# Optimization experiments

Measured on AMD Instinct MI355X. Metric: run time of the kernel, lower is better.

The kernel has to match this reference:

```python
import jax, jax.numpy as jnp
import numpy as np

B, S, D = 2, 192, 256


def _clip_tangent(v, max_norm=4.0):
    n = jnp.linalg.norm(v, axis=-1, keepdims=True) + 1e-8
    return v * jnp.minimum(max_norm / n, 1.0)


def _sq(x):
    return jnp.sum(x * x, axis=-1, keepdims=True)


def _artanh(x):
    return jnp.arctanh(jnp.clip(x, -1.0 + 1e-7, 1.0 - 1e-7))


def _mobius_add(x, y):
    # Poincare ball (c=1) Mobius addition
    x2, y2 = _sq(x), _sq(y)
    xy = jnp.sum(x * y, axis=-1, keepdims=True)
    num = (1.0 + 2.0 * xy + y2) * x + (1.0 - x2) * y
    den = 1.0 + 2.0 * xy + x2 * y2
    return num / jnp.maximum(den, 1e-15)


def _expmap0(v):
    n = jnp.maximum(jnp.linalg.norm(v, axis=-1, keepdims=True), 1e-15)
    return jnp.tanh(n) * v / n


def _logmap0(x):
    n = jnp.maximum(jnp.linalg.norm(x, axis=-1, keepdims=True), 1e-15)
    return _artanh(n) * x / n


def _dist(x, y):
    u = _mobius_add(-x, y)
    return 2.0 * _artanh(jnp.linalg.norm(u, axis=-1))


def _logmap(x, y):
    u = _mobius_add(-x, y)
    un = jnp.maximum(jnp.linalg.norm(u, axis=-1, keepdims=True), 1e-15)
    lam = 2.0 / jnp.maximum(1.0 - _sq(x), 1e-15)
    return (2.0 / lam) * _artanh(un) * u / un


def _expmap(x, v):
    n = jnp.maximum(jnp.linalg.norm(v, axis=-1, keepdims=True), 1e-15)
    lam = 2.0 / jnp.maximum(1.0 - _sq(x), 1e-15)
    return _mobius_add(x, jnp.tanh(lam * n / 2.0) * v / n)


def _projx(x):
    n = jnp.linalg.norm(x, axis=-1, keepdims=True)
    maxn = 1.0 - 1e-5
    return jnp.where(n > maxn, x * maxn / jnp.maximum(n, 1e-15), x)


def _normalize(v, axis, eps=1e-8):
    return v / jnp.maximum(jnp.linalg.norm(v, axis=axis, keepdims=True), eps)


def setup_inputs() -> dict:
    key = jax.random.key(0)
    ks = jax.random.split(key, 8)

    def lin_w(k):
        return 0.02 * jax.random.normal(k, (D, D), jnp.float32)

    return {
        'q_in': 0.1 * jax.random.normal(ks[0], (B, S, D), jnp.float32),
        'k_in': 0.1 * jax.random.normal(ks[1], (B, S, D), jnp.float32),
        'v_in': 0.1 * jax.random.normal(ks[2], (B, S, D), jnp.float32),
        'Wq': lin_w(ks[3]), 'bq': jnp.zeros((D,), jnp.float32),
        'Wk': lin_w(ks[4]), 'bk': jnp.zeros((D,), jnp.float32),
        'Wv': lin_w(ks[5]), 'bv': jnp.zeros((D,), jnp.float32),
        'Wo': lin_w(ks[6]), 'bo': jnp.zeros((D,), jnp.float32),
        'tau': jnp.asarray(0.02, jnp.float32),
        'tangent_scale': jnp.asarray(1.0, jnp.float32),
    }


def _forward(q_in, k_in, v_in, Wq, bq, Wk, bk, Wv, bv, Wo, bo, tau, tangent_scale):
    nk = jax.random.split(jax.random.key(42), 3)  # deterministic stand-in for randn_like noise
    q = q_in @ Wq.T + bq
    k = k_in @ Wk.T + bk
    v = v_in @ Wv.T + bv

    q_hyp = _expmap0(_clip_tangent(q))
    k_hyp = _expmap0(_clip_tangent(k))

    # pairwise hyperbolic distance attention: [B,S,S]
    dist_matrix = _dist(q_hyp[:, :, None, :], k_hyp[:, None, :, :])
    min_dist = jnp.min(dist_matrix, axis=-1, keepdims=True)
    w_unnorm = jnp.exp(-(dist_matrix - min_dist))
    w_probs = w_unnorm / (jnp.sum(w_unnorm, axis=-1, keepdims=True) + 1e-8)
    h = jnp.einsum('bqs,bsd->bqd', w_probs, v)

    # differentiable Karcher flow (3-step Riemannian SGD for Frechet mean)
    wn = w_unnorm / (jnp.sum(w_unnorm, axis=-1, keepdims=True) + 1e-8)
    mu_hyp = _expmap0(_clip_tangent(jnp.einsum('bqs,bsd->bqd', wn, k)))
    k_hyp2 = _expmap0(_clip_tangent(k))
    for _ in range(3):
        log_k = _logmap(mu_hyp[:, :, None, :], k_hyp2[:, None, :, :])  # [B,S,S,D]
        v_grad = jnp.sum(wn[..., None] * log_k, axis=2)
        mu_hyp = _expmap(mu_hyp, _clip_tangent(0.1 * v_grad))

    noise = 1e-5 * jax.random.normal(nk[0], mu_hyp.shape, mu_hyp.dtype)
    k_centroid = _projx(mu_hyp + noise)

    c2k = _dist(k_centroid[:, :, None, :], k_hyp[:, None, :, :])  # [B,S,S]
    wv = w_unnorm / (jnp.sum(w_unnorm, axis=-1, keepdims=True) + 1e-8)
    entropy = -jnp.sum(wv * jnp.log(wv + 1e-8), axis=-1, keepdims=True)
    effective_mass = jnp.exp(entropy)
    variance = jnp.sum(wv * c2k ** 2, axis=-1, keepdims=True)
    tension = variance - tau * effective_mass  # [B,S,1]

    # local tangent frame + power iteration for principal direction
    k_local = _logmap(k_centroid[:, :, None, :], k_hyp[:, None, :, :])  # [B,S,S,D]
    weighted_k = k_local * jnp.sqrt(w_unnorm[..., None] + 1e-8)
    v_rand = jax.random.normal(nk[1], (B, S, D, 1), weighted_k.dtype)
    v_rand = _normalize(v_rand, axis=2)
    for _ in range(3):
        proj = jnp.einsum('bqsd,bqdo->bqso', weighted_k, v_rand)
        v_rand = _normalize(jnp.einsum('bqsd,bqso->bqdo', weighted_k, proj), axis=2)
    w_local = v_rand[..., 0]
    # transp0back(x, v) = v * lambda_x / 2 = v / (1 - ||x||^2)
    w_global = w_local / jnp.maximum(1.0 - _sq(k_centroid), 1e-15)
    fallback = _normalize(_logmap0(q_hyp) - _logmap0(k_centroid), axis=-1)
    w_proj = jnp.where(variance > 1e-5, w_global, fallback)

    h_norm = jnp.linalg.norm(h, axis=-1, keepdims=True)
    h_comp = jnp.arcsinh(h_norm) * h / (h_norm + 1e-8)

    # Pitchfork bifurcation ODE, RK4: dx/dt = tension*x - x^3
    x = jnp.sum(h_comp * w_proj, axis=-1, keepdims=True)
    ode_noise = 1e-4 * jax.random.normal(nk[2], x.shape, x.dtype)
    xi = jnp.where(x == 0, ode_noise, x)
    dt = 0.5
    f = lambda z: tension * z - z ** 3
    for _ in range(4):
        k1 = dt * f(xi)
        k2 = dt * f(xi + k1 / 2)
        k3 = dt * f(xi + k2 / 2)
        k4 = dt * f(xi + k3)
        xi = xi + (k1 + 2 * k2 + 2 * k3 + k4) / 6.0
    h_prime = h_comp + (xi - x) * w_proj
    h_prime_hyp = _expmap0(_clip_tangent(h_prime * tangent_scale))
    h_out_bif = _logmap0(h_prime_hyp)

    tau_safe = jnp.maximum(tau, 1e-3)
    gate = jnp.maximum(jnp.tanh(tension / tau_safe), 0.0)
    h_fused = (1.0 - gate) * h + gate * h_out_bif
    return h_fused @ Wo.T + bo


def reference(q_in, k_in, v_in, Wq, bq, Wk, bk, Wv, bv, Wo, bo, tau, tangent_scale):
    return _forward(q_in, k_in, v_in, Wq, bq, Wk, bk, Wv, bv, Wo, bo, tau, tangent_scale)
```

## Files before the change

kernel.cpp:

```cpp
#include <hip/hip_runtime.h>
#include <hip/hip_bf16.h>
#include <stdint.h>

#define BB 2
#define SS 192
#define DD 256
#define NROW (BB * SS)
#define NE (NROW * DD)

__device__ __forceinline__ uint32_t rotl32(uint32_t v, int d) {
  return (v << d) | (v >> (32 - d));
}

__device__ inline void threefry2x32(uint32_t k0, uint32_t k1, uint32_t x0, uint32_t x1,
                                    uint32_t* o0, uint32_t* o1) {
  uint32_t ks2 = k0 ^ k1 ^ 0x1BD11BDAu;
  x0 += k0; x1 += k1;
  const int ra[4] = {13, 15, 26, 6};
  const int rb[4] = {17, 29, 16, 24};
#pragma unroll
  for (int i = 0; i < 4; i++) { x0 += x1; x1 = rotl32(x1, ra[i]); x1 ^= x0; }
  x0 += k1; x1 += ks2 + 1u;
#pragma unroll
  for (int i = 0; i < 4; i++) { x0 += x1; x1 = rotl32(x1, rb[i]); x1 ^= x0; }
  x0 += ks2; x1 += k0 + 2u;
#pragma unroll
  for (int i = 0; i < 4; i++) { x0 += x1; x1 = rotl32(x1, ra[i]); x1 ^= x0; }
  x0 += k0; x1 += k1 + 3u;
#pragma unroll
  for (int i = 0; i < 4; i++) { x0 += x1; x1 = rotl32(x1, rb[i]); x1 ^= x0; }
  x0 += k1; x1 += ks2 + 4u;
#pragma unroll
  for (int i = 0; i < 4; i++) { x0 += x1; x1 = rotl32(x1, ra[i]); x1 ^= x0; }
  x0 += ks2; x1 += k0 + 5u;
  *o0 = x0; *o1 = x1;
}

__device__ inline float erfinv_xla_f32(float x) {
  float w = -log1pf(-x * x);
  float p;
  if (w < 5.0f) {
    w = w - 2.5f;
    p = 2.81022636e-08f;
    p = 3.43273939e-07f + p * w;
    p = -3.5233877e-06f + p * w;
    p = -4.39150654e-06f + p * w;
    p = 0.00021858087f + p * w;
    p = -0.00125372503f + p * w;
    p = -0.00417768164f + p * w;
    p = 0.246640727f + p * w;
    p = 1.50140941f + p * w;
  } else {
    w = sqrtf(w) - 3.0f;
    p = -0.000200214257f;
    p = 0.000100950558f + p * w;
    p = 0.00134934322f + p * w;
    p = -0.00367342844f + p * w;
    p = 0.00573950773f + p * w;
    p = -0.0076224613f + p * w;
    p = 0.00943887047f + p * w;
    p = 1.00167406f + p * w;
    p = 2.83297682f + p * w;
  }
  return p * x;
}

__device__ inline float jax_normal_from_bits(uint32_t bits) {
  float f = __uint_as_float((bits >> 9) | 0x3f800000u) - 1.0f;
  const float lo = -0.99999994f;
  float u = f * (1.0f - lo) + lo;
  u = fmaxf(lo, u);
  return 1.4142135623730951f * erfinv_xla_f32(u);
}

__device__ inline float jax_normal_at(uint32_t ka, uint32_t kb, uint32_t i) {
  uint32_t o0, o1;
  threefry2x32(ka, kb, 0u, i, &o0, &o1);
  return jax_normal_from_bits(o0 ^ o1);
}

__device__ inline double blockSum(double v, double* red, int tid) {
#pragma unroll
  for (int o = 32; o > 0; o >>= 1) v += __shfl_down(v, o, 64);
  __syncthreads();
  if ((tid & 63) == 0) red[tid >> 6] = v;
  __syncthreads();
  return (red[0] + red[1]) + (red[2] + red[3]);
}

__device__ inline double reduceS_sum(const double* arr, double* red, int tid) {
  __syncthreads();
  if (tid < 64) {
    double v = arr[tid] + arr[tid + 64] + arr[tid + 128];
#pragma unroll
    for (int o = 32; o > 0; o >>= 1) v += __shfl_down(v, o, 64);
    if (tid == 0) red[4] = v;
  }
  __syncthreads();
  return red[4];
}

__device__ inline double reduceS_min(const double* arr, double* red, int tid) {
  __syncthreads();
  if (tid < 64) {
    double v = fmin(arr[tid], fmin(arr[tid + 64], arr[tid + 128]));
#pragma unroll
    for (int o = 32; o > 0; o >>= 1) v = fmin(v, __shfl_down(v, o, 64));
    if (tid == 0) red[5] = v;
  }
  __syncthreads();
  return red[5];
}

#define SDOT(vecLds, khTp, outv) do {                                        \
    const float* cb_ = (khTp) + tid;                                         \
    double s0_=0.0,s1_=0.0,s2_=0.0,s3_=0.0,s4_=0.0,s5_=0.0,s6_=0.0,s7_=0.0;  \
    for (int d0_ = 0; d0_ < DD; d0_ += 8) {                                  \
      float f0_ = cb_[(size_t)(d0_ + 0) * SS];                               \
      float f1_ = cb_[(size_t)(d0_ + 1) * SS];                               \
      float f2_ = cb_[(size_t)(d0_ + 2) * SS];                               \
      float f3_ = cb_[(size_t)(d0_ + 3) * SS];                               \
      float f4_ = cb_[(size_t)(d0_ + 4) * SS];                               \
      float f5_ = cb_[(size_t)(d0_ + 5) * SS];                               \
      float f6_ = cb_[(size_t)(d0_ + 6) * SS];                               \
      float f7_ = cb_[(size_t)(d0_ + 7) * SS];                               \
      s0_ += (vecLds)[d0_ + 0] * (double)f0_;                                \
      s1_ += (vecLds)[d0_ + 1] * (double)f1_;                                \
      s2_ += (vecLds)[d0_ + 2] * (double)f2_;                                \
      s3_ += (vecLds)[d0_ + 3] * (double)f3_;                                \
      s4_ += (vecLds)[d0_ + 4] * (double)f4_;                                \
      s5_ += (vecLds)[d0_ + 5] * (double)f5_;                                \
      s6_ += (vecLds)[d0_ + 6] * (double)f6_;                                \
      s7_ += (vecLds)[d0_ + 7] * (double)f7_;                                \
    }                                                                        \
    (outv) = ((s0_ + s1_) + (s2_ + s3_)) + ((s4_ + s5_) + (s6_ + s7_));      \
  } while (0)

#define DSUM(wArr, mat, outv) do {                                           \
    const float* mb_ = (mat) + tid;                                          \
    double s0_=0.0,s1_=0.0,s2_=0.0,s3_=0.0,s4_=0.0,s5_=0.0,s6_=0.0,s7_=0.0;  \
    for (int t0_ = 0; t0_ < SS; t0_ += 8) {                                  \
      float f0_ = mb_[(size_t)(t0_ + 0) * DD];                               \
      float f1_ = mb_[(size_t)(t0_ + 1) * DD];                               \
      float f2_ = mb_[(size_t)(t0_ + 2) * DD];                               \
      float f3_ = mb_[(size_t)(t0_ + 3) * DD];                               \
      float f4_ = mb_[(size_t)(t0_ + 4) * DD];                               \
      float f5_ = mb_[(size_t)(t0_ + 5) * DD];                               \
      float f6_ = mb_[(size_t)(t0_ + 6) * DD];                               \
      float f7_ = mb_[(size_t)(t0_ + 7) * DD];                               \
      s0_ += (wArr)[t0_ + 0] * (double)f0_;                                  \
      s1_ += (wArr)[t0_ + 1] * (double)f1_;                                  \
      s2_ += (wArr)[t0_ + 2] * (double)f2_;                                  \
      s3_ += (wArr)[t0_ + 3] * (double)f3_;                                  \
      s4_ += (wArr)[t0_ + 4] * (double)f4_;                                  \
      s5_ += (wArr)[t0_ + 5] * (double)f5_;                                  \
      s6_ += (wArr)[t0_ + 6] * (double)f6_;                                  \
      s7_ += (wArr)[t0_ + 7] * (double)f7_;                                  \
    }                                                                        \
    (outv) = ((s0_ + s1_) + (s2_ + s3_)) + ((s4_ + s5_) + (s6_ + s7_));      \
  } while (0)

__global__ void transpose4(const float* __restrict__ Wq, const float* __restrict__ Wk,
                           const float* __restrict__ Wv, const float* __restrict__ Wo,
                           float* __restrict__ WqT, float* __restrict__ WkT,
                           float* __restrict__ WvT, float* __restrict__ WoT) {
  int m = blockIdx.x >> 8;
  int i = blockIdx.x & 255;
  int j = threadIdx.x;
  const float* S_; float* D_;
  if (m == 0) { S_ = Wq; D_ = WqT; }
  else if (m == 1) { S_ = Wk; D_ = WkT; }
  else if (m == 2) { S_ = Wv; D_ = WvT; }
  else { S_ = Wo; D_ = WoT; }
  D_[i * DD + j] = S_[j * DD + i];
}

__device__ inline double colDot(const float* __restrict__ xs,
                                const float* __restrict__ WT, int j) {
  const float* cb = WT + j;
  double s0=0.0,s1=0.0,s2=0.0,s3=0.0,s4=0.0,s5=0.0,s6=0.0,s7=0.0;
  for (int i0 = 0; i0 < DD; i0 += 8) {
    float f0 = cb[(size_t)(i0 + 0) * DD];
    float f1 = cb[(size_t)(i0 + 1) * DD];
    float f2 = cb[(size_t)(i0 + 2) * DD];
    float f3 = cb[(size_t)(i0 + 3) * DD];
    float f4 = cb[(size_t)(i0 + 4) * DD];
    float f5 = cb[(size_t)(i0 + 5) * DD];
    float f6 = cb[(size_t)(i0 + 6) * DD];
    float f7 = cb[(size_t)(i0 + 7) * DD];
    s0 += (double)xs[i0 + 0] * (double)f0;
    s1 += (double)xs[i0 + 1] * (double)f1;
    s2 += (double)xs[i0 + 2] * (double)f2;
    s3 += (double)xs[i0 + 3] * (double)f3;
    s4 += (double)xs[i0 + 4] * (double)f4;
    s5 += (double)xs[i0 + 5] * (double)f5;
    s6 += (double)xs[i0 + 6] * (double)f6;
    s7 += (double)xs[i0 + 7] * (double)f7;
  }
  return ((s0 + s1) + (s2 + s3)) + ((s4 + s5) + (s6 + s7));
}

__global__ __launch_bounds__(256) void proj_kernel(
    const float* __restrict__ q_in, const float* __restrict__ k_in, const float* __restrict__ v_in,
    const float* __restrict__ WqT, const float* __restrict__ WkT, const float* __restrict__ WvT,
    const float* __restrict__ bq, const float* __restrict__ bk, const float* __restrict__ bv,
    float* __restrict__ qh, float* __restrict__ kb, float* __restrict__ vb,
    float* __restrict__ kh, float* __restrict__ khT, double* __restrict__ y2g) {
  const int row = blockIdx.x, m = blockIdx.y, j = threadIdx.x;
  __shared__ float xs[DD];
  __shared__ double red[8];
  const float* x; const float* WT; const float* bias;
  if (m == 0) { x = q_in; WT = WqT; bias = bq; }
  else if (m == 1) { x = k_in; WT = WkT; bias = bk; }
  else { x = v_in; WT = WvT; bias = bv; }
  xs[j] = x[(size_t)row * DD + j];
  __syncthreads();
  double val = colDot(xs, WT, j) + (double)bias[j];

  if (m == 2) { vb[(size_t)row * DD + j] = (float)val; return; }

  double n2 = blockSum(val * val, red, j);
  double n = sqrt(n2);
  double cf = fmin(4.0 / (n + 1e-8), 1.0);
  double ncl = fmax(n * cf, 1e-15);
  double sc = tanh(ncl) * cf / ncl;
  if (m == 0) {
    qh[(size_t)row * DD + j] = (float)(val * sc);
  } else {
    kb[(size_t)row * DD + j] = (float)val;
    float khf = (float)(val * sc);
    kh[(size_t)row * DD + j] = khf;
    int bb = row / SS, s = row % SS;
    khT[((size_t)bb * DD + j) * SS + s] = khf;
    double y2 = blockSum((double)khf * (double)khf, red, j);
    if (j == 0) y2g[row] = y2;
  }
}

__global__ __launch_bounds__(256) void gemm_out(
    const float* __restrict__ hf, const float* __restrict__ WoT,
    const float* __restrict__ bo, float* __restrict__ out) {
  int row = blockIdx.x;
  int j = threadIdx.x;
  __shared__ float xs[DD];
  xs[j] = hf[(size_t)row * DD + j];
  __syncthreads();
  out[(size_t)row * DD + j] = (float)(colDot(xs, WoT, j) + (double)bo[j]);
}

__global__ __launch_bounds__(256) void resonance_main(
    const float* __restrict__ q_hyp, const float* __restrict__ k_hyp,
    const float* __restrict__ k_hypT, const float* __restrict__ kmat,
    const float* __restrict__ vmat, const double* __restrict__ y2g,
    const float* __restrict__ tau_p, const float* __restrict__ ts_p,
    float* __restrict__ hfused) {
  __shared__ double xq[DD], xc[DD], vr[DD];
  __shared__ double y2s[SS], wun[SS], wns[SS], alf[SS], bet[SS], sA[SS], sB[SS];
  __shared__ double red[8];
  const int tid = threadIdx.x;
  const int blk = blockIdx.x;
  const int b = blk / SS;
  const size_t rowOff = (size_t)blk * DD;
  const float* khB = k_hyp + (size_t)b * SS * DD;
  const float* khT = k_hypT + (size_t)b * DD * SS;
  const float* kB = kmat + (size_t)b * SS * DD;
  const float* vB = vmat + (size_t)b * SS * DD;

  uint32_t nk0a, nk0b, nk1a, nk1b, nk2a, nk2b;
  threefry2x32(0u, 42u, 0u, 0u, &nk0a, &nk0b);
  threefry2x32(0u, 42u, 0u, 1u, &nk1a, &nk1b);
  threefry2x32(0u, 42u, 0u, 2u, &nk2a, &nk2b);
  const uint32_t ei = (uint32_t)(rowOff + tid);
  const double noiseval = 1e-5 * (double)jax_normal_at(nk0a, nk0b, ei);
  const double vrndval = (double)jax_normal_at(nk1a, nk1b, ei);
  const double odeval = 1e-4 * (double)jax_normal_at(nk2a, nk2b, (uint32_t)blk);

  double xqv = (double)q_hyp[rowOff + tid];
  xq[tid] = xqv;
  if (tid < SS) y2s[tid] = y2g[b * SS + tid];
  double x2q = blockSum(xqv * xqv, red, tid);

  if (tid < SS) {
    double dot;
    SDOT(xq, khT, dot);
    double y2 = y2s[tid];
    double A = 1.0 - 2.0 * dot + y2;
    double Dn = fmax(1.0 - 2.0 * dot + x2q * y2, 1e-15);
    double Bc = 1.0 - x2q;
    double u2 = (A * A * x2q - 2.0 * A * Bc * dot + Bc * Bc * y2) / (Dn * Dn);
    double unr = sqrt(fmax(u2, 0.0));
    sA[tid] = 2.0 * atanh(fmin(unr, 1.0 - 1e-7));
  }
  double mind = reduceS_min(sA, red, tid);
  if (tid < SS) wun[tid] = exp(-(sA[tid] - mind));
  double wsum = reduceS_sum(wun, red, tid);
  if (tid < SS) wns[tid] = wun[tid] * (1.0 / (wsum + 1e-8));
  __syncthreads();

  double hreg, mu;
  {
    const float* vb_ = vB + tid;
    const float* kb_ = kB + tid;
    double h0=0.0,h1=0.0,h2=0.0,h3=0.0, m0=0.0,m1=0.0,m2=0.0,m3=0.0;
    for (int s0 = 0; s0 < SS; s0 += 4) {
      float v0 = vb_[(size_t)(s0 + 0) * DD];
      float v1 = vb_[(size_t)(s0 + 1) * DD];
      float v2 = vb_[(size_t)(s0 + 2) * DD];
      float v3 = vb_[(size_t)(s0 + 3) * DD];
      float k0 = kb_[(size_t)(s0 + 0) * DD];
      float k1 = kb_[(size_t)(s0 + 1) * DD];
      float k2 = kb_[(size_t)(s0 + 2) * DD];
      float k3 = kb_[(size_t)(s0 + 3) * DD];
      double w0 = wns[s0 + 0], w1 = wns[s0 + 1], w2 = wns[s0 + 2], w3 = wns[s0 + 3];
      h0 += w0 * (double)v0; h1 += w1 * (double)v1;
      h2 += w2 * (double)v2; h3 += w3 * (double)v3;
      m0 += w0 * (double)k0; m1 += w1 * (double)k1;
      m2 += w2 * (double)k2; m3 += w3 * (double)k3;
    }
    hreg = (h0 + h1) + (h2 + h3);
    mu = (m0 + m1) + (m2 + m3);
  }

  double x2c;
  {
    double n2 = blockSum(mu * mu, red, tid);
    double n = sqrt(n2);
    double cf = fmin(4.0 / (n + 1e-8), 1.0);
    double ncl = fmax(n * cf, 1e-15);
    double th = tanh(ncl);
    xc[tid] = mu * (th * cf / ncl);
    x2c = th * th;
  }
  __syncthreads();

  for (int it = 0; it < 3; ++it) {
    if (tid < SS) {
      double dot;
      SDOT(xc, khT, dot);
      double y2 = y2s[tid];
      double A = 1.0 - 2.0 * dot + y2;
      double Dn = fmax(1.0 - 2.0 * dot + x2c * y2, 1e-15);
      double Bc = 1.0 - x2c;
      double u2 = (A * A * x2c - 2.0 * A * Bc * dot + Bc * Bc * y2) / (Dn * Dn);
      double unr = sqrt(fmax(u2, 0.0));
      double un = fmax(unr, 1e-15);
      double coef = fmax(Bc, 1e-15) * atanh(fmin(un, 1.0 - 1e-7)) / un;
      double cs = wns[tid] * coef / Dn;
      sA[tid] = cs;
      sB[tid] = cs * A;
    }
    double S1 = reduceS_sum(sB, red, tid);
    double g;
    DSUM(sA, khB, g);
    double xold = xc[tid];
    double Bc = 1.0 - x2c;
    double vg = Bc * g - S1 * xold;
    double nv2 = blockSum(vg * vg, red, tid);
    double nv = 0.1 * sqrt(nv2);
    double cf = fmin(4.0 / (nv + 1e-8), 1.0);
    double nw = fmax(nv * cf, 1e-15);
    double tsc = tanh(nw / fmax(Bc, 1e-15));
    double zco = tsc * 0.1 * cf / nw;
    double z = zco * vg;
    double xz = blockSum(xold * z, red, tid);
    double z2 = tsc * tsc;
    double den = fmax(1.0 + 2.0 * xz + x2c * z2, 1e-15);
    double xnew = ((1.0 + 2.0 * xz + z2) * xold + (1.0 - x2c) * z) / den;
    xc[tid] = xnew;
    x2c = blockSum(xnew * xnew, red, tid);
  }

  {
    double cn = xc[tid] + noiseval;
    double n2 = blockSum(cn * cn, red, tid);
    double nn = sqrt(n2);
    if (nn > 1.0 - 1e-5) cn *= (1.0 - 1e-5) / fmax(nn, 1e-15);
    xc[tid] = cn;
    x2c = blockSum(cn * cn, red, tid);
  }

  if (tid < SS) {
    double dot;
    SDOT(xc, khT, dot);
    double y2 = y2s[tid];
    double A = 1.0 - 2.0 * dot + y2;
    double Dn = fmax(1.0 - 2.0 * dot + x2c * y2, 1e-15);
    double Bc = 1.0 - x2c;
    double u2 = (A * A * x2c - 2.0 * A * Bc * dot + Bc * Bc * y2) / (Dn * Dn);
    double unr = sqrt(fmax(u2, 0.0));
    double c2k = 2.0 * atanh(fmin(unr, 1.0 - 1e-7));
    sA[tid] = wns[tid] * c2k * c2k;
    sB[tid] = -wns[tid] * log(wns[tid] + 1e-8);
    double un = fmax(unr, 1e-15);
    double gl = fmax(Bc, 1e-15) * atanh(fmin(un, 1.0 - 1e-7)) / (un * Dn);
    double sq = sqrt(wun[tid] + 1e-8);
    alf[tid] = -sq * gl * A;
    bet[tid] = sq * gl * Bc;
  }
  double variance = reduceS_sum(sA, red, tid);
  double entropy = reduceS_sum(sB, red, tid);
  double tau = (double)tau_p[0];
  double tension = variance - tau * exp(entropy);

  {
    double n2 = blockSum(vrndval * vrndval, red, tid);
    vr[tid] = vrndval / fmax(sqrt(n2), 1e-8);
  }
  for (int it = 0; it < 3; ++it) {
    double dxv = blockSum(xc[tid] * vr[tid], red, tid);
    if (tid < SS) {
      double dot;
      SDOT(vr, khT, dot);
      double pj = alf[tid] * dxv + bet[tid] * dot;
      sA[tid] = alf[tid] * pj;
      sB[tid] = bet[tid] * pj;
    }
    double T1 = reduceS_sum(sA, red, tid);
    double g;
    DSUM(sB, khB, g);
    double vnew = T1 * xc[tid] + g;
    double n2 = blockSum(vnew * vnew, red, tid);
    vr[tid] = vnew / fmax(sqrt(n2), 1e-8);
  }

  double wproj;
  {
    double wg = vr[tid] / fmax(1.0 - x2c, 1e-15);
    double nq = fmax(sqrt(x2q), 1e-15);
    double aq = atanh(fmin(nq, 1.0 - 1e-7)) / nq;
    double nc = fmax(sqrt(x2c), 1e-15);
    double ac = atanh(fmin(nc, 1.0 - 1e-7)) / nc;
    double f = aq * xq[tid] - ac * xc[tid];
    double n2 = blockSum(f * f, red, tid);
    double fb = f / fmax(sqrt(n2), 1e-8);
    wproj = (variance > 1e-5) ? wg : fb;
  }

  double hn2 = blockSum(hreg * hreg, red, tid);
  double hn = sqrt(hn2);
  double hsc = asinh(hn) / (hn + 1e-8);
  double hc = hsc * hreg;
  double x = blockSum(hc * wproj, red, tid);
  double xi = (x == 0.0) ? odeval : x;
  const double dt = 0.5;
#pragma unroll
  for (int r = 0; r < 4; ++r) {
    double k1 = dt * (tension * xi - xi * xi * xi);
    double a2 = xi + 0.5 * k1;
    double k2 = dt * (tension * a2 - a2 * a2 * a2);
    double a3 = xi + 0.5 * k2;
    double k3 = dt * (tension * a3 - a3 * a3 * a3);
    double a4 = xi + k3;
    double k4 = dt * (tension * a4 - a4 * a4 * a4);
    xi += (k1 + 2.0 * k2 + 2.0 * k3 + k4) / 6.0;
  }
  double ts = (double)ts_p[0];
  double hp = (hc + (xi - x) * wproj) * ts;
  double hp2 = blockSum(hp * hp, red, tid);
  double nhp = sqrt(hp2);
  double cf = fmin(4.0 / (nhp + 1e-8), 1.0);
  double ncl = fmax(nhp * cf, 1e-15);
  double th = tanh(ncl);
  double nb = fmax(th, 1e-15);
  double ab = atanh(fmin(nb, 1.0 - 1e-7)) / nb;
  double hob = ab * th * cf / ncl * hp;
  double gate = fmax(tanh(tension / fmax(tau, 1e-3)), 0.0);
  hfused[rowOff + tid] = (float)((1.0 - gate) * hreg + gate * hob);
}

extern "C" void kernel_launch(void* const* d_in, const int* in_sizes, int n_in,
                              void* d_out, int out_size, void* d_ws, size_t ws_size,
                              hipStream_t stream) {
  const float* q_in = (const float*)d_in[0];
  const float* k_in = (const float*)d_in[1];
  const float* v_in = (const float*)d_in[2];
  const float* Wq = (const float*)d_in[3];
  const float* bq = (const float*)d_in[4];
  const float* Wk = (const float*)d_in[5];
  const float* bk = (const float*)d_in[6];
  const float* Wv = (const float*)d_in[7];
  const float* bv = (const float*)d_in[8];
  const float* Wo = (const float*)d_in[9];
  const float* bo = (const float*)d_in[10];
  const float* tau = (const float*)d_in[11];
  const float* ts = (const float*)d_in[12];
  float* out = (float*)d_out;
  (void)in_sizes; (void)n_in; (void)out_size; (void)ws_size;

  char* base = (char*)d_ws;
  size_t off = 0;
  auto alloc = [&](size_t bytes) -> void* {
    void* p = base + off;
    off += (bytes + 255) & ~(size_t)255;
    return p;
  };
  float* WqT = (float*)alloc((size_t)DD * DD * 4);
  float* WkT = (float*)alloc((size_t)DD * DD * 4);
  float* WvT = (float*)alloc((size_t)DD * DD * 4);
  float* WoT = (float*)alloc((size_t)DD * DD * 4);
  float* kb = (float*)alloc((size_t)NE * 4);
  float* vb = (float*)alloc((size_t)NE * 4);
  float* qh = (float*)alloc((size_t)NE * 4);
  float* kh = (float*)alloc((size_t)NE * 4);
  float* khT = (float*)alloc((size_t)NE * 4);
  double* y2g = (double*)alloc((size_t)NROW * 8);
  float* hf = (float*)alloc((size_t)NE * 4);

  hipLaunchKernelGGL(transpose4, dim3(4 * DD), dim3(DD), 0, stream,
                     Wq, Wk, Wv, Wo, WqT, WkT, WvT, WoT);
  hipLaunchKernelGGL(proj_kernel, dim3(NROW, 3), dim3(DD), 0, stream,
                     q_in, k_in, v_in, WqT, WkT, WvT, bq, bk, bv,
                     qh, kb, vb, kh, khT, y2g);
  hipLaunchKernelGGL(resonance_main, dim3(NROW), dim3(DD), 0, stream,
                     qh, kh, khT, kb, vb, y2g, tau, ts, hf);
  hipLaunchKernelGGL(gemm_out, dim3(NROW), dim3(DD), 0, stream, hf, WoT, bo, out);
}
```

Before: 146.3 us.

## Use float4-packed transposed keys and fuse output projection into main kernel

The transposed key matrix is now stored in groups of four consecutive features as float4, built with wave shuffles in the projection kernel. The score dot products then read 16-byte vectors and double2 values from LDS instead of scalar strided loads. The separate output GEMM kernel is removed: each resonance block writes its fused row to LDS and computes the Wo projection itself, saving a launch and a global round trip. The per-accumulator summation order changes slightly, and the fused tail adds work to an already long per-row kernel.

```diff
diff --git a/kernel.cpp b/kernel.cpp
--- a/kernel.cpp
+++ b/kernel.cpp
@@ -112,32 +112,40 @@
   return red[5];
 }
 
-#define SDOT(vecLds, khTp, outv) do {                                        \
-    const float* cb_ = (khTp) + tid;                                         \
-    double s0_=0.0,s1_=0.0,s2_=0.0,s3_=0.0,s4_=0.0,s5_=0.0,s6_=0.0,s7_=0.0;  \
-    for (int d0_ = 0; d0_ < DD; d0_ += 8) {                                  \
-      float f0_ = cb_[(size_t)(d0_ + 0) * SS];                               \
-      float f1_ = cb_[(size_t)(d0_ + 1) * SS];                               \
-      float f2_ = cb_[(size_t)(d0_ + 2) * SS];                               \
-      float f3_ = cb_[(size_t)(d0_ + 3) * SS];                               \
-      float f4_ = cb_[(size_t)(d0_ + 4) * SS];                               \
-      float f5_ = cb_[(size_t)(d0_ + 5) * SS];                               \
-      float f6_ = cb_[(size_t)(d0_ + 6) * SS];                               \
-      float f7_ = cb_[(size_t)(d0_ + 7) * SS];                               \
-      s0_ += (vecLds)[d0_ + 0] * (double)f0_;                                \
-      s1_ += (vecLds)[d0_ + 1] * (double)f1_;                                \
-      s2_ += (vecLds)[d0_ + 2] * (double)f2_;                                \
-      s3_ += (vecLds)[d0_ + 3] * (double)f3_;                                \
-      s4_ += (vecLds)[d0_ + 4] * (double)f4_;                                \
-      s5_ += (vecLds)[d0_ + 5] * (double)f5_;                                \
-      s6_ += (vecLds)[d0_ + 6] * (double)f6_;                                \
-      s7_ += (vecLds)[d0_ + 7] * (double)f7_;                                \
-    }                                                                        \
-    (outv) = ((s0_ + s1_) + (s2_ + s3_)) + ((s4_ + s5_) + (s6_ + s7_));      \
-  } while (0)
+__device__ inline double sdot4(const double* __restrict__ vec, const float4* __restrict__ cb) {
+  const double2* vp = (const double2*)vec;
+  double A0=0,A1=0,A2=0,A3=0,A4=0,A5=0,A6=0,A7=0;
+  for (int g = 0; g < DD / 4; g += 8) {
+    float4 f0 = cb[(size_t)(g + 0) * SS];
+    float4 f1 = cb[(size_t)(g + 1) * SS];
+    float4 f2 = cb[(size_t)(g + 2) * SS];
+    float4 f3 = cb[(size_t)(g + 3) * SS];
+    float4 f4 = cb[(size_t)(g + 4) * SS];
+    float4 f5 = cb[(size_t)(g + 5) * SS];
+    float4 f6 = cb[(size_t)(g + 6) * SS];
+    float4 f7 = cb[(size_t)(g + 7) * SS];
+    { double2 a = vp[2*(g+0)], b = vp[2*(g+0)+1];
+      A0 += a.x*(double)f0.x; A0 += a.y*(double)f0.y; A0 += b.x*(double)f0.z; A0 += b.y*(double)f0.w; }
+    { double2 a = vp[2*(g+1)], b = vp[2*(g+1)+1];
+      A1 += a.x*(double)f1.x; A1 += a.y*(double)f1.y; A1 += b.x*(double)f1.z; A1 += b.y*(double)f1.w; }
+    { double2 a = vp[2*(g+2)], b = vp[2*(g+2)+1];
+      A2 += a.x*(double)f2.x; A2 += a.y*(double)f2.y; A2 += b.x*(double)f2.z; A2 += b.y*(double)f2.w; }
+    { double2 a = vp[2*(g+3)], b = vp[2*(g+3)+1];
+      A3 += a.x*(double)f3.x; A3 += a.y*(double)f3.y; A3 += b.x*(double)f3.z; A3 += b.y*(double)f3.w; }
+    { double2 a = vp[2*(g+4)], b = vp[2*(g+4)+1];
+      A4 += a.x*(double)f4.x; A4 += a.y*(double)f4.y; A4 += b.x*(double)f4.z; A4 += b.y*(double)f4.w; }
+    { double2 a = vp[2*(g+5)], b = vp[2*(g+5)+1];
+      A5 += a.x*(double)f5.x; A5 += a.y*(double)f5.y; A5 += b.x*(double)f5.z; A5 += b.y*(double)f5.w; }
+    { double2 a = vp[2*(g+6)], b = vp[2*(g+6)+1];
+      A6 += a.x*(double)f6.x; A6 += a.y*(double)f6.y; A6 += b.x*(double)f6.z; A6 += b.y*(double)f6.w; }
+    { double2 a = vp[2*(g+7)], b = vp[2*(g+7)+1];
+      A7 += a.x*(double)f7.x; A7 += a.y*(double)f7.y; A7 += b.x*(double)f7.z; A7 += b.y*(double)f7.w; }
+  }
+  return ((A0 + A1) + (A2 + A3)) + ((A4 + A5) + (A6 + A7));
+}
 
 #define DSUM(wArr, mat, outv) do {                                           \
-    const float* mb_ = (mat) + tid;                                          \
+    const float* mb_ = (mat);                                                \
     double s0_=0.0,s1_=0.0,s2_=0.0,s3_=0.0,s4_=0.0,s5_=0.0,s6_=0.0,s7_=0.0;  \
     for (int t0_ = 0; t0_ < SS; t0_ += 8) {                                  \
       float f0_ = mb_[(size_t)(t0_ + 0) * DD];                               \
@@ -205,7 +213,7 @@
     const float* __restrict__ WqT, const float* __restrict__ WkT, const float* __restrict__ WvT,
     const float* __restrict__ bq, const float* __restrict__ bk, const float* __restrict__ bv,
     float* __restrict__ qh, float* __restrict__ kb, float* __restrict__ vb,
-    float* __restrict__ kh, float* __restrict__ khT, double* __restrict__ y2g) {
+    float* __restrict__ kh, float4* __restrict__ khT4, double* __restrict__ y2g) {
   const int row = blockIdx.x, m = blockIdx.y, j = threadIdx.x;
   __shared__ float xs[DD];
   __shared__ double red[8];
@@ -230,39 +238,34 @@
     kb[(size_t)row * DD + j] = (float)val;
     float khf = (float)(val * sc);
     kh[(size_t)row * DD + j] = khf;
+    float h1 = __shfl_down(khf, 1, 64);
+    float h2 = __shfl_down(khf, 2, 64);
+    float h3 = __shfl_down(khf, 3, 64);
     int bb = row / SS, s = row % SS;
-    khT[((size_t)bb * DD + j) * SS + s] = khf;
+    if (!(j & 3))
+      khT4[((size_t)bb * (DD / 4) + (j >> 2)) * SS + s] = make_float4(khf, h1, h2, h3);
     double y2 = blockSum((double)khf * (double)khf, red, j);
     if (j == 0) y2g[row] = y2;
   }
 }
 
-__global__ __launch_bounds__(256) void gemm_out(
-    const float* __restrict__ hf, const float* __restrict__ WoT,
-    const float* __restrict__ bo, float* __restrict__ out) {
-  int row = blockIdx.x;
-  int j = threadIdx.x;
-  __shared__ float xs[DD];
-  xs[j] = hf[(size_t)row * DD + j];
-  __syncthreads();
-  out[(size_t)row * DD + j] = (float)(colDot(xs, WoT, j) + (double)bo[j]);
-}
-
 __global__ __launch_bounds__(256) void resonance_main(
     const float* __restrict__ q_hyp, const float* __restrict__ k_hyp,
-    const float* __restrict__ k_hypT, const float* __restrict__ kmat,
+    const float4* __restrict__ khT4, const float* __restrict__ kmat,
     const float* __restrict__ vmat, const double* __restrict__ y2g,
+    const float* __restrict__ WoT, const float* __restrict__ bo,
     const float* __restrict__ tau_p, const float* __restrict__ ts_p,
-    float* __restrict__ hfused) {
-  __shared__ double xq[DD], xc[DD], vr[DD];
+    float* __restrict__ out) {
+  __shared__ __align__(16) double xq[DD], xc[DD], vr[DD];
   __shared__ double y2s[SS], wun[SS], wns[SS], alf[SS], bet[SS], sA[SS], sB[SS];
+  __shared__ float hfl[DD];
   __shared__ double red[8];
   const int tid = threadIdx.x;
   const int blk = blockIdx.x;
   const int b = blk / SS;
   const size_t rowOff = (size_t)blk * DD;
   const float* khB = k_hyp + (size_t)b * SS * DD;
-  const float* khT = k_hypT + (size_t)b * DD * SS;
+  const float4* khT4B = khT4 + (size_t)b * (DD / 4) * SS + tid;
   const float* kB = kmat + (size_t)b * SS * DD;
   const float* vB = vmat + (size_t)b * SS * DD;
 
@@ -281,8 +284,7 @@
   double x2q = blockSum(xqv * xqv, red, tid);
 
   if (tid < SS) {
-    double dot;
-    SDOT(xq, khT, dot);
+    double dot = sdot4(xq, khT4B);
     double y2 = y2s[tid];
     double A = 1.0 - 2.0 * dot + y2;
     double Dn = fmax(1.0 - 2.0 * dot + x2q * y2, 1e-15);
@@ -335,8 +337,7 @@
 
   for (int it = 0; it < 3; ++it) {
     if (tid < SS) {
-      double dot;
-      SDOT(xc, khT, dot);
+      double dot = sdot4(xc, khT4B);
       double y2 = y2s[tid];
       double A = 1.0 - 2.0 * dot + y2;
       double Dn = fmax(1.0 - 2.0 * dot + x2c * y2, 1e-15);
@@ -351,7 +352,7 @@
     }
     double S1 = reduceS_sum(sB, red, tid);
     double g;
-    DSUM(sA, khB, g);
+    DSUM(sA, khB + tid, g);
     double xold = xc[tid];
     double Bc = 1.0 - x2c;
     double vg = Bc * g - S1 * xold;
@@ -380,8 +381,7 @@
   }
 
   if (tid < SS) {
-    double dot;
-    SDOT(xc, khT, dot);
+    double dot = sdot4(xc, khT4B);
     double y2 = y2s[tid];
     double A = 1.0 - 2.0 * dot + y2;
     double Dn = fmax(1.0 - 2.0 * dot + x2c * y2, 1e-15);
@@ -409,15 +409,14 @@
   for (int it = 0; it < 3; ++it) {
     double dxv = blockSum(xc[tid] * vr[tid], red, tid);
     if (tid < SS) {
-      double dot;
-      SDOT(vr, khT, dot);
+      double dot = sdot4(vr, khT4B);
       double pj = alf[tid] * dxv + bet[tid] * dot;
       sA[tid] = alf[tid] * pj;
       sB[tid] = bet[tid] * pj;
     }
     double T1 = reduceS_sum(sA, red, tid);
     double g;
-    DSUM(sB, khB, g);
+    DSUM(sB, khB + tid, g);
     double vnew = T1 * xc[tid] + g;
     double n2 = blockSum(vnew * vnew, red, tid);
     vr[tid] = vnew / fmax(sqrt(n2), 1e-8);
@@ -465,7 +464,11 @@
   double ab = atanh(fmin(nb, 1.0 - 1e-7)) / nb;
   double hob = ab * th * cf / ncl * hp;
   double gate = fmax(tanh(tension / fmax(tau, 1e-3)), 0.0);
-  hfused[rowOff + tid] = (float)((1.0 - gate) * hreg + gate * hob);
+
+  hfl[tid] = (float)((1.0 - gate) * hreg + gate * hob);
+  __syncthreads();
+  double o = colDot(hfl, WoT, tid) + (double)bo[tid];
+  out[rowOff + tid] = (float)o;
 }
 
 extern "C" void kernel_launch(void* const* d_in, const int* in_sizes, int n_in,
@@ -502,16 +505,14 @@
   float* vb = (float*)alloc((size_t)NE * 4);
   float* qh = (float*)alloc((size_t)NE * 4);
   float* kh = (float*)alloc((size_t)NE * 4);
-  float* khT = (float*)alloc((size_t)NE * 4);
+  float4* khT4 = (float4*)alloc((size_t)NE * 4);
   double* y2g = (double*)alloc((size_t)NROW * 8);
-  float* hf = (float*)alloc((size_t)NE * 4);
 
   hipLaunchKernelGGL(transpose4, dim3(4 * DD), dim3(DD), 0, stream,
                      Wq, Wk, Wv, Wo, WqT, WkT, WvT, WoT);
   hipLaunchKernelGGL(proj_kernel, dim3(NROW, 3), dim3(DD), 0, stream,
                      q_in, k_in, v_in, WqT, WkT, WvT, bq, bk, bv,
-                     qh, kb, vb, kh, khT, y2g);
+                     qh, kb, vb, kh, khT4, y2g);
   hipLaunchKernelGGL(resonance_main, dim3(NROW), dim3(DD), 0, stream,
-                     qh, kh, khT, kb, vb, y2g, tau, ts, hf);
-  hipLaunchKernelGGL(gemm_out, dim3(NROW), dim3(DD), 0, stream, hf, WoT, bo, out);
-}
+                     qh, kh, khT4, kb, vb, y2g, WoT, bo, tau, ts, out);
+}
```

Result: slower. 195.9 us (+34.0%).
